# Kernel tuning notes

Measured on AMD Instinct MI355X. Metric: run time of the kernel, lower is better.

Reference implementation:

```python
import jax, jax.numpy as jnp
import numpy as np
from jax import lax

VOCAB = 32000; D = 1024; NL = 4; DI = 2048; S = 16; R = 64; DC = 4
B = 1; L = 1024; EPS = 1e-5


def setup_inputs() -> dict:
    key = jax.random.key(0)
    ks = jax.random.split(key, 16)
    def n(k, shape, s=0.02):
        return jax.random.normal(k, shape, dtype=jnp.float32) * s
    return dict(
        tokens=jax.random.randint(ks[0], (B, L), 0, VOCAB),
        embed=n(ks[1], (VOCAB, D)),
        norm_w=jnp.ones((NL, D), jnp.float32) + n(ks[2], (NL, D)),
        in_proj_w=n(ks[3], (NL, 2 * DI, D)),
        conv_w=n(ks[4], (NL, DI, DC), 0.1),
        conv_b=n(ks[5], (NL, DI)),
        x_proj_w=n(ks[6], (NL, R + 2 * S, DI)),
        dt_proj_w=n(ks[7], (NL, DI, R), 0.1),
        dt_proj_b=n(ks[8], (NL, DI), 0.5),
        A_log=n(ks[9], (NL, DI, S), 0.5),
        D_param=jnp.ones((NL, DI), jnp.float32) + n(ks[10], (NL, DI)),
        out_proj_w=n(ks[11], (NL, D, DI)),
        norm_f_w=jnp.ones((D,), jnp.float32),
        lm_head_w=n(ks[12], (VOCAB, D)),
    )


def _rmsnorm(x, w):
    return x * lax.rsqrt(jnp.mean(x * x, axis=-1, keepdims=True) + EPS) * w


def _mamba_block(x, norm_w, in_w, cw, cb, xw, dtw, dtb, a_log, dp, ow):
    # x: [B, L, D]
    res = x
    x = _rmsnorm(x, norm_w)
    xz = jnp.einsum('bld,ed->ble', x, in_w)      # [B, L, 2*DI]
    u, z = xz[..., :DI], xz[..., DI:]
    # depthwise causal conv over time
    u = jnp.swapaxes(u, 1, 2)                    # [B, DI, L]
    u = lax.conv_general_dilated(u, cw[:, None, :], (1,), [(DC - 1, 0)],
                                 feature_group_count=DI,
                                 dimension_numbers=('NCH', 'OIH', 'NCH'))
    u = jax.nn.silu(u + cb[None, :, None])
    u = jnp.swapaxes(u, 1, 2)                    # [B, L, DI]
    # input-dependent SSM params
    dbc = jnp.einsum('bld,ed->ble', u, xw)       # [B, L, R+2S]
    dt = jax.nn.softplus(jnp.einsum('blr,dr->bld', dbc[..., :R], dtw) + dtb)
    Bm = dbc[..., R:R + S]                       # [B, L, S]
    Cm = dbc[..., R + S:]                        # [B, L, S]
    A = -jnp.exp(a_log)                          # [DI, S]
    dA = jnp.exp(dt[..., None] * A)              # [B, L, DI, S]
    dBu = (dt * u)[..., None] * Bm[:, :, None, :]  # [B, L, DI, S]
    # selective scan over time
    def step(h, inp):
        a_t, b_t, c_t = inp
        h = a_t * h + b_t                        # [B, DI, S]
        y = jnp.einsum('bds,bs->bd', h, c_t)
        return h, y
    h0 = jnp.zeros((x.shape[0], DI, S), x.dtype)
    _, ys = lax.scan(step, h0, (jnp.moveaxis(dA, 1, 0), jnp.moveaxis(dBu, 1, 0), jnp.moveaxis(Cm, 1, 0)))
    y = jnp.moveaxis(ys, 0, 1) + u * dp          # [B, L, DI]
    y = y * jax.nn.silu(z)
    return res + jnp.einsum('bld,od->blo', y, ow)


def reference(tokens, embed, norm_w, in_proj_w, conv_w, conv_b, x_proj_w,
              dt_proj_w, dt_proj_b, A_log, D_param, out_proj_w, norm_f_w, lm_head_w):
    x = embed[tokens]                            # [B, L, D]
    for i in range(NL):
        x = _mamba_block(x, norm_w[i], in_proj_w[i], conv_w[i], conv_b[i],
                         x_proj_w[i], dt_proj_w[i], dt_proj_b[i], A_log[i],
                         D_param[i], out_proj_w[i])
    x = _rmsnorm(x, norm_f_w)
    return jnp.einsum('bld,vd->blv', x, lm_head_w)  # [B, L, VOCAB]
```

## Files before the change

### kernel.cpp

```cpp
#include <hip/hip_runtime.h>
#include <hip/hip_bf16.h>
#include <math.h>


typedef __attribute__((ext_vector_type(8))) short bf16x8;
typedef __attribute__((ext_vector_type(4))) float f32x4;

__device__ __forceinline__ short f2bf(float f) {
  union { float f; unsigned u; } v; v.f = f;
  unsigned u = v.u;
  unsigned r = (u + 0x7FFFu + ((u >> 16) & 1u)) >> 16;
  return (short)r;
}

__device__ __forceinline__ bf16x8 pack8(float4 a, float4 b) {
  bf16x8 r;
  r[0] = f2bf(a.x); r[1] = f2bf(a.y); r[2] = f2bf(a.z); r[3] = f2bf(a.w);
  r[4] = f2bf(b.x); r[5] = f2bf(b.y); r[6] = f2bf(b.z); r[7] = f2bf(b.w);
  return r;
}

__device__ __forceinline__ unsigned cvtpk(float lo, float hi) {
  unsigned r;
  asm("v_cvt_pk_bf16_f32 %0, %1, %2" : "=v"(r) : "v"(lo), "v"(hi));
  return r;
}

__device__ __forceinline__ float softplus_f(float x) {
  return (x > 20.f) ? x : log1pf(__expf(x));
}

__device__ __forceinline__ void gl_lds16(const void* g, void* l) {
  void* gnc = (void*)g;
  __builtin_amdgcn_global_load_lds((__attribute__((address_space(1))) void*)gnc,
                                   (__attribute__((address_space(3))) void*)l, 16, 0, 0);
}

__global__ __launch_bounds__(256) void cvt4_k(const float* __restrict__ s0, unsigned short* __restrict__ d0, int nb0,
                                              const float* __restrict__ s1, unsigned short* __restrict__ d1, int nb1,
                                              const float* __restrict__ s2, unsigned short* __restrict__ d2, int nb2,
                                              const float* __restrict__ s3, unsigned short* __restrict__ d3, int nb3) {
  int b = blockIdx.x;
  const float* s; unsigned short* d; int lb;
  if (b < nb0) { s = s0; d = d0; lb = b; }
  else if (b < nb0 + nb1) { s = s1; d = d1; lb = b - nb0; }
  else if (b < nb0 + nb1 + nb2) { s = s2; d = d2; lb = b - nb0 - nb1; }
  else { s = s3; d = d3; lb = b - nb0 - nb1 - nb2; }
  size_t base = (size_t)lb * 1024;
#pragma unroll
  for (int u = 0; u < 4; ++u) {
    size_t idx = base + u * 256 + threadIdx.x;
    const float4* p = (const float4*)(s + idx * 8);
    float4 a = p[0], bq = p[1];
    uint4 w;
    w.x = cvtpk(a.x, a.y); w.y = cvtpk(a.z, a.w);
    w.z = cvtpk(bq.x, bq.y); w.w = cvtpk(bq.z, bq.w);
    *(uint4*)(d + idx * 8) = w;
  }
}

__global__ __launch_bounds__(256) void embed_rms_k(const int* __restrict__ tok,
                                                   const float* __restrict__ emb,
                                                   const float* __restrict__ w,
                                                   float* __restrict__ x,
                                                   unsigned short* __restrict__ xn16) {
  int l = blockIdx.x;
  int t = tok[l];
  float4 v = ((const float4*)(emb + (size_t)t * 1024))[threadIdx.x];
  ((float4*)(x + (size_t)l * 1024))[threadIdx.x] = v;
  float ss = v.x * v.x + v.y * v.y + v.z * v.z + v.w * v.w;
  ss += __shfl_down(ss, 32); ss += __shfl_down(ss, 16); ss += __shfl_down(ss, 8);
  ss += __shfl_down(ss, 4);  ss += __shfl_down(ss, 2);  ss += __shfl_down(ss, 1);
  __shared__ float wsum[4];
  if ((threadIdx.x & 63) == 0) wsum[threadIdx.x >> 6] = ss;
  __syncthreads();
  float tot = wsum[0] + wsum[1] + wsum[2] + wsum[3];
  float sc = rsqrtf(tot * (1.0f / 1024.0f) + 1e-5f);
  float4 wv = ((const float4*)w)[threadIdx.x];
  ushort4 o;
  o.x = (unsigned short)f2bf(v.x * sc * wv.x);
  o.y = (unsigned short)f2bf(v.y * sc * wv.y);
  o.z = (unsigned short)f2bf(v.z * sc * wv.z);
  o.w = (unsigned short)f2bf(v.w * sc * wv.w);
  *(ushort4*)(xn16 + (size_t)l * 1024 + threadIdx.x * 4) = o;
}

__global__ __launch_bounds__(256) void rmsnorm16_k(const float* __restrict__ x,
                                                   const float* __restrict__ w,
                                                   unsigned short* __restrict__ y) {
  int l = blockIdx.x;
  const float4* xr = (const float4*)(x + (size_t)l * 1024);
  float4 v = xr[threadIdx.x];
  float ss = v.x * v.x + v.y * v.y + v.z * v.z + v.w * v.w;
  ss += __shfl_down(ss, 32); ss += __shfl_down(ss, 16); ss += __shfl_down(ss, 8);
  ss += __shfl_down(ss, 4);  ss += __shfl_down(ss, 2);  ss += __shfl_down(ss, 1);
  __shared__ float wsum[4];
  if ((threadIdx.x & 63) == 0) wsum[threadIdx.x >> 6] = ss;
  __syncthreads();
  float tot = wsum[0] + wsum[1] + wsum[2] + wsum[3];
  float sc = rsqrtf(tot * (1.0f / 1024.0f) + 1e-5f);
  float4 wv = ((const float4*)w)[threadIdx.x];
  ushort4 o;
  o.x = (unsigned short)f2bf(v.x * sc * wv.x);
  o.y = (unsigned short)f2bf(v.y * sc * wv.y);
  o.z = (unsigned short)f2bf(v.z * sc * wv.z);
  o.w = (unsigned short)f2bf(v.w * sc * wv.w);
  *(ushort4*)(y + (size_t)l * 1024 + threadIdx.x * 4) = o;
}

__global__ __launch_bounds__(256) void rmsnorm_k(const float* __restrict__ x,
                                                 const float* __restrict__ w,
                                                 float* __restrict__ y) {
  int l = blockIdx.x;
  const float4* xr = (const float4*)(x + (size_t)l * 1024);
  float4 v = xr[threadIdx.x];
  float ss = v.x * v.x + v.y * v.y + v.z * v.z + v.w * v.w;
  ss += __shfl_down(ss, 32); ss += __shfl_down(ss, 16); ss += __shfl_down(ss, 8);
  ss += __shfl_down(ss, 4);  ss += __shfl_down(ss, 2);  ss += __shfl_down(ss, 1);
  __shared__ float wsum[4];
  if ((threadIdx.x & 63) == 0) wsum[threadIdx.x >> 6] = ss;
  __syncthreads();
  float tot = wsum[0] + wsum[1] + wsum[2] + wsum[3];
  float sc = rsqrtf(tot * (1.0f / 1024.0f) + 1e-5f);
  float4 wv = ((const float4*)w)[threadIdx.x];
  float4 o;
  o.x = v.x * sc * wv.x; o.y = v.y * sc * wv.y;
  o.z = v.z * sc * wv.z; o.w = v.w * sc * wv.w;
  ((float4*)(y + (size_t)l * 1024))[threadIdx.x] = o;
}

__global__ __launch_bounds__(256) void conv_silu_k(const float* __restrict__ xz,
                                                   const float* __restrict__ cw,
                                                   const float* __restrict__ cb,
                                                   float* __restrict__ u,
                                                   unsigned short* __restrict__ u16) {
  int idx = blockIdx.x * 256 + threadIdx.x;
  int d = idx & 2047;
  int l = idx >> 11;
  float acc = cb[d];
#pragma unroll
  for (int j = 0; j < 4; ++j) {
    int ll = l - 3 + j;
    if (ll >= 0) acc = fmaf(xz[(size_t)ll * 4096 + d], cw[d * 4 + j], acc);
  }
  float sig = 1.0f / (1.0f + __expf(-acc));
  float v = acc * sig;
  u[idx] = v;
  if (u16) u16[idx] = (unsigned short)f2bf(v);
}

__global__ __launch_bounds__(256) void gemm16_k(const unsigned short* __restrict__ A, int lda,
                                                const unsigned short* __restrict__ W, int ldw,
                                                const float* __restrict__ addsrc,
                                                const float* __restrict__ spbias,
                                                float* __restrict__ C, int ldc,
                                                unsigned short* __restrict__ C16,
                                                int gx, int N, int K) {
  int total = gridDim.x;
  int lin = blockIdx.x;
  int q = total >> 3, r = total & 7;
  int xcd = lin & 7, idx = lin >> 3;
  int nl = (xcd < r ? xcd * (q + 1) : r * (q + 1) + (xcd - r) * q) + idx;
  const int bm = (nl % gx) << 7;
  const int bn = (nl / gx) << 7;

  const int tid = threadIdx.x;
  const int wid = tid >> 6;
  const int lane = tid & 63;
  const int wm = (wid >> 1) << 6;
  const int wn = (wid & 1) << 6;
  const int fr = lane & 15;
  const int kg = lane >> 4;
  const int srow = lane >> 3;
  const int sch  = lane & 7;
  const int xch  = sch ^ srow;

  __shared__ unsigned short sA[2][8192];
  __shared__ unsigned short sB[2][8192];

  f32x4 acc[4][4];
#pragma unroll
  for (int i = 0; i < 4; ++i)
#pragma unroll
    for (int j = 0; j < 4; ++j) acc[i][j] = (f32x4){0.f, 0.f, 0.f, 0.f};

  auto STAGE = [&](int b, int k0) {
#pragma unroll
    for (int t = 0; t < 4; ++t) {
      int g = (wid << 2) + t;
      int row = (g << 3) + srow;
      const unsigned short* ga = A + (size_t)(bm + row) * lda + k0 + (xch << 3);
      int wrow = bn + row; if (wrow >= N) wrow = N - 1;
      const unsigned short* gw = W + (size_t)wrow * ldw + k0 + (xch << 3);
      gl_lds16(ga, &sA[b][g << 9]);
      gl_lds16(gw, &sB[b][g << 9]);
    }
  };

  auto COMPUTE = [&](int b) {
#pragma unroll
    for (int ks = 0; ks < 2; ++ks) {
      bf16x8 af[4], bw[4];
#pragma unroll
      for (int mi = 0; mi < 4; ++mi) {
        int row = wm + (mi << 4) + fr;
        int xc = ((ks << 2) + kg) ^ (fr & 7);
        af[mi] = *(const bf16x8*)&sA[b][(row << 6) + (xc << 3)];
      }
#pragma unroll
      for (int ni = 0; ni < 4; ++ni) {
        int row = wn + (ni << 4) + fr;
        int xc = ((ks << 2) + kg) ^ (fr & 7);
        bw[ni] = *(const bf16x8*)&sB[b][(row << 6) + (xc << 3)];
      }
#pragma unroll
      for (int mi = 0; mi < 4; ++mi)
#pragma unroll
        for (int ni = 0; ni < 4; ++ni)
          acc[mi][ni] = __builtin_amdgcn_mfma_f32_16x16x32_bf16(af[mi], bw[ni], acc[mi][ni], 0, 0, 0);
    }
  };

  const int nt = K >> 6;
  STAGE(0, 0);
  int cur = 0;
  for (int t = 0; t + 1 < nt; ++t) {
    STAGE(cur ^ 1, (t + 1) << 6);
    asm volatile("s_waitcnt vmcnt(8)" ::: "memory");
    __builtin_amdgcn_s_barrier();
    __builtin_amdgcn_sched_barrier(0);
    COMPUTE(cur);
    __builtin_amdgcn_s_barrier();
    cur ^= 1;
  }
  asm volatile("s_waitcnt vmcnt(0)" ::: "memory");
  __builtin_amdgcn_s_barrier();
  __builtin_amdgcn_sched_barrier(0);
  COMPUTE(cur);

#pragma unroll
  for (int mi = 0; mi < 4; ++mi)
#pragma unroll
    for (int ni = 0; ni < 4; ++ni) {
      int n = bn + wn + (ni << 4) + fr;
      if (n < N) {
#pragma unroll
        for (int i = 0; i < 4; ++i) {
          int m = bm + wm + (mi << 4) + (kg << 2) + i;
          size_t off = (size_t)m * ldc + n;
          float v = acc[mi][ni][i];
          if (addsrc) v += addsrc[off];
          if (spbias) v = softplus_f(v + spbias[n]);
          C[off] = v;
          if (C16) C16[off] = (unsigned short)f2bf(v);
        }
      }
    }
}

__global__ __launch_bounds__(256) void gemm16sk_k(const unsigned short* __restrict__ A, int lda,
                                                  const unsigned short* __restrict__ W, int ldw,
                                                  float* __restrict__ Cp, int ldc,
                                                  int gx, int N, int Kchunk, int Mtot) {
  int total = gridDim.x;
  int lin = blockIdx.x;
  int q = total >> 3, r = total & 7;
  int xcd = lin & 7, idx = lin >> 3;
  int nl = (xcd < r ? xcd * (q + 1) : r * (q + 1) + (xcd - r) * q) + idx;
  const int bm = (nl % gx) << 7;
  const int bn = (nl / gx) << 7;
  const int ksplit = blockIdx.y;
  const int kbase = ksplit * Kchunk;

  const int tid = threadIdx.x;
  const int wid = tid >> 6;
  const int lane = tid & 63;
  const int wm = (wid >> 1) << 6;
  const int wn = (wid & 1) << 6;
  const int fr = lane & 15;
  const int kg = lane >> 4;
  const int srow = lane >> 3;
  const int sch  = lane & 7;
  const int xch  = sch ^ srow;

  __shared__ unsigned short sA[2][8192];
  __shared__ unsigned short sB[2][8192];

  f32x4 acc[4][4];
#pragma unroll
  for (int i = 0; i < 4; ++i)
#pragma unroll
    for (int j = 0; j < 4; ++j) acc[i][j] = (f32x4){0.f, 0.f, 0.f, 0.f};

  auto STAGE = [&](int b, int k0) {
#pragma unroll
    for (int t = 0; t < 4; ++t) {
      int g = (wid << 2) + t;
      int row = (g << 3) + srow;
      const unsigned short* ga = A + (size_t)(bm + row) * lda + k0 + (xch << 3);
      int wrow = bn + row; if (wrow >= N) wrow = N - 1;
      const unsigned short* gw = W + (size_t)wrow * ldw + k0 + (xch << 3);
      gl_lds16(ga, &sA[b][g << 9]);
      gl_lds16(gw, &sB[b][g << 9]);
    }
  };

  auto COMPUTE = [&](int b) {
#pragma unroll
    for (int ks = 0; ks < 2; ++ks) {
      bf16x8 af[4], bw[4];
#pragma unroll
      for (int mi = 0; mi < 4; ++mi) {
        int row = wm + (mi << 4) + fr;
        int xc = ((ks << 2) + kg) ^ (fr & 7);
        af[mi] = *(const bf16x8*)&sA[b][(row << 6) + (xc << 3)];
      }
#pragma unroll
      for (int ni = 0; ni < 4; ++ni) {
        int row = wn + (ni << 4) + fr;
        int xc = ((ks << 2) + kg) ^ (fr & 7);
        bw[ni] = *(const bf16x8*)&sB[b][(row << 6) + (xc << 3)];
      }
#pragma unroll
      for (int mi = 0; mi < 4; ++mi)
#pragma unroll
        for (int ni = 0; ni < 4; ++ni)
          acc[mi][ni] = __builtin_amdgcn_mfma_f32_16x16x32_bf16(af[mi], bw[ni], acc[mi][ni], 0, 0, 0);
    }
  };

  const int nt = Kchunk >> 6;
  STAGE(0, kbase);
  int cur = 0;
  for (int t = 0; t + 1 < nt; ++t) {
    STAGE(cur ^ 1, kbase + ((t + 1) << 6));
    asm volatile("s_waitcnt vmcnt(8)" ::: "memory");
    __builtin_amdgcn_s_barrier();
    __builtin_amdgcn_sched_barrier(0);
    COMPUTE(cur);
    __builtin_amdgcn_s_barrier();
    cur ^= 1;
  }
  asm volatile("s_waitcnt vmcnt(0)" ::: "memory");
  __builtin_amdgcn_s_barrier();
  __builtin_amdgcn_sched_barrier(0);
  COMPUTE(cur);

  float* Cs = Cp + (size_t)ksplit * Mtot * ldc;
#pragma unroll
  for (int mi = 0; mi < 4; ++mi)
#pragma unroll
    for (int ni = 0; ni < 4; ++ni) {
      int n = bn + wn + (ni << 4) + fr;
      if (n < N) {
#pragma unroll
        for (int i = 0; i < 4; ++i) {
          int m = bm + wm + (mi << 4) + (kg << 2) + i;
          Cs[(size_t)m * ldc + n] = acc[mi][ni][i];
        }
      }
    }
}

__global__ __launch_bounds__(256) void reduce_xp_k(const float* __restrict__ Cp,
                                                   float* __restrict__ dbc,
                                                   unsigned short* __restrict__ dbc16) {
  int i = blockIdx.x * 256 + threadIdx.x;
  float v = Cp[i] + Cp[98304 + i] + Cp[2 * 98304 + i] + Cp[3 * 98304 + i];
  dbc[i] = v;
  dbc16[i] = (unsigned short)f2bf(v);
}

__global__ __launch_bounds__(256) void reduce_op_k(const float* __restrict__ Cp,
                                                   float* __restrict__ x) {
  int i = blockIdx.x * 256 + threadIdx.x;
  const float4* p0 = (const float4*)Cp;
  const float4* p1 = (const float4*)(Cp + 1048576);
  const float4* p2 = (const float4*)(Cp + 2097152);
  const float4* p3 = (const float4*)(Cp + 3145728);
  float4 a = p0[i], b = p1[i], c = p2[i], d = p3[i];
  float4 xv = ((float4*)x)[i];
  xv.x += a.x + b.x + c.x + d.x;
  xv.y += a.y + b.y + c.y + d.y;
  xv.z += a.z + b.z + c.z + d.z;
  xv.w += a.w + b.w + c.w + d.w;
  ((float4*)x)[i] = xv;
}

struct WREG { float4 v[8]; };

__global__ __launch_bounds__(512, 2) void gemm256f_k(const unsigned short* __restrict__ A, int lda,
                                                     const float* __restrict__ W, int ldw,
                                                     float* __restrict__ C, int ldc,
                                                     int gx, int N, int K) {
  int total = gridDim.x;
  int lin = blockIdx.x;
  int q = total >> 3, r = total & 7;
  int xcd = lin & 7, idx = lin >> 3;
  int nl = (xcd < r ? xcd * (q + 1) : r * (q + 1) + (xcd - r) * q) + idx;
  const int bm = (nl % gx) << 8;
  const int bn = (nl / gx) << 8;

  const int tid = threadIdx.x;
  const int wid = tid >> 6;
  const int lane = tid & 63;
  const int wm = (wid >> 2) << 7;
  const int wn = (wid & 3) << 6;
  const int fr = lane & 15;
  const int kg = lane >> 4;
  const int srow = lane >> 3;
  const int sch  = lane & 7;
  const int xch  = sch ^ srow;

  const int wr_row  = tid >> 1;
  const int wr_half = tid & 1;
  int wr_grow = bn + wr_row; if (wr_grow >= N) wr_grow = N - 1;
  const float* gWrow = W + (size_t)wr_grow * ldw + wr_half * 32;

  __shared__ unsigned short sA[2][16384];
  __shared__ unsigned short sB[2][16384];

  f32x4 acc[8][4];
#pragma unroll
  for (int i = 0; i < 8; ++i)
#pragma unroll
    for (int j = 0; j < 4; ++j) acc[i][j] = (f32x4){0.f, 0.f, 0.f, 0.f};

  auto STAGE_A = [&](unsigned short* buf, int k0) {
#pragma unroll
    for (int t = 0; t < 4; ++t) {
      int g = (wid << 2) + t;
      int row = (g << 3) + srow;
      const unsigned short* ga = A + (size_t)(bm + row) * lda + k0 + (xch << 3);
      gl_lds16(ga, &buf[g << 9]);
    }
  };

  WREG wr;
  auto WLOAD = [&](int k0) {
    const float4* p = (const float4*)(gWrow + k0);
#pragma unroll
    for (int j = 0; j < 8; ++j) wr.v[j] = p[j];
  };

  auto WWRITE = [&](unsigned short* buf) {
#pragma unroll
    for (int c2 = 0; c2 < 4; ++c2) {
      int c = (wr_half << 2) + c2;
      uint4 val;
      val.x = cvtpk(wr.v[2 * c2].x,     wr.v[2 * c2].y);
      val.y = cvtpk(wr.v[2 * c2].z,     wr.v[2 * c2].w);
      val.z = cvtpk(wr.v[2 * c2 + 1].x, wr.v[2 * c2 + 1].y);
      val.w = cvtpk(wr.v[2 * c2 + 1].z, wr.v[2 * c2 + 1].w);
      *(uint4*)&buf[(wr_row << 6) + ((c ^ (wr_row & 7)) << 3)] = val;
    }
  };

  auto COMPUTE = [&](const unsigned short* bufa, const unsigned short* bufb) {
#pragma unroll
    for (int ks = 0; ks < 2; ++ks) {
      bf16x8 af[8], bw[4];
#pragma unroll
      for (int mi = 0; mi < 8; ++mi) {
        int row = wm + (mi << 4) + fr;
        int xc = ((ks << 2) + kg) ^ (fr & 7);
        af[mi] = *(const bf16x8*)&bufa[(row << 6) + (xc << 3)];
      }
#pragma unroll
      for (int ni = 0; ni < 4; ++ni) {
        int row = wn + (ni << 4) + fr;
        int xc = ((ks << 2) + kg) ^ (fr & 7);
        bw[ni] = *(const bf16x8*)&bufb[(row << 6) + (xc << 3)];
      }
#pragma unroll
      for (int mi = 0; mi < 8; ++mi)
#pragma unroll
        for (int ni = 0; ni < 4; ++ni)
          acc[mi][ni] = __builtin_amdgcn_mfma_f32_16x16x32_bf16(af[mi], bw[ni], acc[mi][ni], 0, 0, 0);
    }
  };

  const int nt = K >> 6;

  STAGE_A(sA[0], 0);
  WLOAD(0);
  asm volatile("s_waitcnt vmcnt(0)" ::: "memory");
  __builtin_amdgcn_sched_barrier(0);
  WWRITE(sB[0]);
  asm volatile("s_waitcnt lgkmcnt(0)" ::: "memory");
  __builtin_amdgcn_s_barrier();
  __builtin_amdgcn_sched_barrier(0);

  int cur = 0;
  for (int t = 0; t < nt; ++t) {
    if (t + 1 < nt) {
      STAGE_A(sA[cur ^ 1], (t + 1) << 6);
      WLOAD((t + 1) << 6);
      __builtin_amdgcn_sched_barrier(0);
    }
    COMPUTE(sA[cur], sB[cur]);
    __builtin_amdgcn_s_barrier();
    if (t + 1 < nt) {
      asm volatile("s_waitcnt vmcnt(0)" ::: "memory");
      __builtin_amdgcn_sched_barrier(0);
      WWRITE(sB[cur ^ 1]);
      asm volatile("s_waitcnt lgkmcnt(0)" ::: "memory");
      __builtin_amdgcn_s_barrier();
      __builtin_amdgcn_sched_barrier(0);
      cur ^= 1;
    }
  }

#pragma unroll
  for (int mi = 0; mi < 8; ++mi)
#pragma unroll
    for (int ni = 0; ni < 4; ++ni) {
      int n = bn + wn + (ni << 4) + fr;
      if (n < N) {
#pragma unroll
        for (int i = 0; i < 4; ++i) {
          int m = bm + wm + (mi << 4) + (kg << 2) + i;
          C[(size_t)m * ldc + n] = acc[mi][ni][i];
        }
      }
    }
}

__global__ __launch_bounds__(256) void gemm_bt_k(const float* __restrict__ A, int lda,
                                                 const float* __restrict__ W, int ldw,
                                                 const float* __restrict__ addsrc,
                                                 float* __restrict__ C, int ldc,
                                                 int N, int K) {
  const int tid  = threadIdx.x;
  const int srow = tid >> 1;
  const int skg  = (tid & 1) << 1;
  const int bm = blockIdx.x << 7;
  const int bn = blockIdx.y << 7;
  const int wid = tid >> 6;
  const int lane = tid & 63;
  const int wm = (wid >> 1) << 6;
  const int wn = (wid & 1) << 6;
  const int fr = lane & 15;
  const int kg = lane >> 4;

  __shared__ bf16x8 lA[4][128];
  __shared__ bf16x8 lB[4][128];

  f32x4 zero4 = {0.f, 0.f, 0.f, 0.f};
  f32x4 acc[4][4];
#pragma unroll
  for (int i = 0; i < 4; ++i)
#pragma unroll
    for (int j = 0; j < 4; ++j) acc[i][j] = zero4;

  const bool wvalid = (bn + srow) < N;
  const float* gA = A + (size_t)(bm + srow) * lda + (skg << 3);
  const float* gW = W + (size_t)(wvalid ? (bn + srow) : 0) * ldw + (skg << 3);

  for (int k0 = 0; k0 < K; k0 += 32) {
    float4 a0 = *(const float4*)(gA + k0);
    float4 a1 = *(const float4*)(gA + k0 + 4);
    float4 a2 = *(const float4*)(gA + k0 + 8);
    float4 a3 = *(const float4*)(gA + k0 + 12);
    float4 w0 = make_float4(0.f, 0.f, 0.f, 0.f), w1 = w0, w2 = w0, w3 = w0;
    if (wvalid) {
      w0 = *(const float4*)(gW + k0);
      w1 = *(const float4*)(gW + k0 + 4);
      w2 = *(const float4*)(gW + k0 + 8);
      w3 = *(const float4*)(gW + k0 + 12);
    }
    __syncthreads();
    lA[skg][srow]     = pack8(a0, a1);
    lA[skg + 1][srow] = pack8(a2, a3);
    lB[skg][srow]     = pack8(w0, w1);
    lB[skg + 1][srow] = pack8(w2, w3);
    __syncthreads();

    bf16x8 af[4], bf_[4];
#pragma unroll
    for (int mi = 0; mi < 4; ++mi) af[mi] = lA[kg][wm + (mi << 4) + fr];
#pragma unroll
    for (int ni = 0; ni < 4; ++ni) bf_[ni] = lB[kg][wn + (ni << 4) + fr];
#pragma unroll
    for (int mi = 0; mi < 4; ++mi)
#pragma unroll
      for (int ni = 0; ni < 4; ++ni)
        acc[mi][ni] = __builtin_amdgcn_mfma_f32_16x16x32_bf16(af[mi], bf_[ni], acc[mi][ni], 0, 0, 0);
  }

#pragma unroll
  for (int mi = 0; mi < 4; ++mi)
#pragma unroll
    for (int ni = 0; ni < 4; ++ni) {
      int n = bn + wn + (ni << 4) + fr;
      if (n < N) {
#pragma unroll
        for (int i = 0; i < 4; ++i) {
          int m = bm + wm + (mi << 4) + (kg << 2) + i;
          size_t off = (size_t)m * ldc + n;
          float v = acc[mi][ni][i];
          if (addsrc) v += addsrc[off];
          C[off] = v;
        }
      }
    }
}

#define NCH 32
#define CHL 32

__global__ __launch_bounds__(256) void scan_p1f_k(const float* __restrict__ dtv,
                                                  const float* __restrict__ u,
                                                  const float* __restrict__ dbc,
                                                  const float* __restrict__ A_log,
                                                  float* __restrict__ Pg,
                                                  float* __restrict__ qg) {
  int tid = threadIdx.x;
  int s = tid & 15, dg = tid >> 4;
  int d = (blockIdx.x << 4) + dg;
  int c = blockIdx.y;
  int l0 = c << 5;
  float A = -__expf(A_log[d * 16 + s]);
  float P = 1.f, q = 0.f;
#pragma unroll 4
  for (int i = 0; i < CHL; ++i) {
    int l = l0 + i;
    size_t rd = (size_t)l * 2048 + d;
    float dt = dtv[rd];
    float dA = __expf(dt * A);
    P *= dA;
    q = fmaf(dA, q, dt * u[rd] * dbc[l * 96 + 64 + s]);
  }
  size_t o = (size_t)c * 32768 + d * 16 + s;
  Pg[o] = P;
  qg[o] = q;
}

__global__ __launch_bounds__(256) void scan_p3f_k(const float* __restrict__ dtv,
                                                  const float* __restrict__ u,
                                                  const float* __restrict__ dbc,
                                                  const float* __restrict__ xz,
                                                  const float* __restrict__ A_log,
                                                  const float* __restrict__ Dp,
                                                  const float* __restrict__ Pg,
                                                  const float* __restrict__ qg,
                                                  unsigned short* __restrict__ y16) {
  int tid = threadIdx.x;
  int s = tid & 15, dg = tid >> 4;
  int d = (blockIdx.x << 4) + dg;
  int c = blockIdx.y;
  int l0 = c << 5;
  float A = -__expf(A_log[d * 16 + s]);
  float dpar = Dp[d];
  float h = 0.f;
  for (int cc = 0; cc < c; ++cc) {
    size_t o = (size_t)cc * 32768 + d * 16 + s;
    h = fmaf(Pg[o], h, qg[o]);
  }
#pragma unroll 4
  for (int i = 0; i < CHL; ++i) {
    int l = l0 + i;
    size_t rd = (size_t)l * 2048 + d;
    float dt = dtv[rd];
    float uv = u[rd];
    float dA = __expf(dt * A);
    h = fmaf(dA, h, dt * uv * dbc[l * 96 + 64 + s]);
    float p = h * dbc[l * 96 + 80 + s];
    p += __shfl_xor(p, 1); p += __shfl_xor(p, 2);
    p += __shfl_xor(p, 4); p += __shfl_xor(p, 8);
    if (s == 0) {
      float zv = xz[(size_t)l * 4096 + 2048 + d];
      float sig = 1.0f / (1.0f + __expf(-zv));
      y16[rd] = (unsigned short)f2bf((p + uv * dpar) * (zv * sig));
    }
  }
}

__global__ __launch_bounds__(256) void scan_p1_k(const float* __restrict__ dtr,
                                                 const float* __restrict__ u,
                                                 const float* __restrict__ dbc,
                                                 const float* __restrict__ A_log,
                                                 const float* __restrict__ dtb,
                                                 float* __restrict__ Pg,
                                                 float* __restrict__ qg) {
  int tid = threadIdx.x;
  int s = tid & 15, dg = tid >> 4;
  int d = (blockIdx.x << 4) + dg;
  int c = blockIdx.y;
  int l0 = c << 5;
  float A = -__expf(A_log[d * 16 + s]);
  float bias = dtb[d];
  float P = 1.f, q = 0.f;
#pragma unroll 4
  for (int i = 0; i < CHL; ++i) {
    int l = l0 + i;
    float dt = softplus_f(dtr[(size_t)l * 2048 + d] + bias);
    float dA = __expf(dt * A);
    P *= dA;
    q = fmaf(dA, q, dt * u[(size_t)l * 2048 + d] * dbc[l * 96 + 64 + s]);
  }
  size_t o = (size_t)c * 32768 + d * 16 + s;
  Pg[o] = P;
  qg[o] = q;
}

__global__ __launch_bounds__(256) void scan_p2_k(const float* __restrict__ Pg,
                                                 const float* __restrict__ qg,
                                                 float* __restrict__ hst) {
  int idx = blockIdx.x * 256 + threadIdx.x;
  float h = 0.f;
#pragma unroll
  for (int c = 0; c < NCH; ++c) {
    size_t o = (size_t)c * 32768 + idx;
    hst[o] = h;
    h = fmaf(Pg[o], h, qg[o]);
  }
}

__global__ __launch_bounds__(256) void scan_p3_k(const float* __restrict__ dtr,
                                                 const float* __restrict__ u,
                                                 const float* __restrict__ dbc,
                                                 const float* __restrict__ xz,
                                                 const float* __restrict__ A_log,
                                                 const float* __restrict__ Dp,
                                                 const float* __restrict__ dtb,
                                                 const float* __restrict__ hst,
                                                 float* __restrict__ y) {
  int tid = threadIdx.x;
  int s = tid & 15, dg = tid >> 4;
  int d = (blockIdx.x << 4) + dg;
  int c = blockIdx.y;
  int l0 = c << 5;
  float A = -__expf(A_log[d * 16 + s]);
  float dpar = Dp[d];
  float bias = dtb[d];
  float h = hst[(size_t)c * 32768 + d * 16 + s];
#pragma unroll 4
  for (int i = 0; i < CHL; ++i) {
    int l = l0 + i;
    size_t rd = (size_t)l * 2048 + d;
    float dt = softplus_f(dtr[rd] + bias);
    float uv = u[rd];
    float dA = __expf(dt * A);
    h = fmaf(dA, h, dt * uv * dbc[l * 96 + 64 + s]);
    float p = h * dbc[l * 96 + 80 + s];
    p += __shfl_xor(p, 1); p += __shfl_xor(p, 2);
    p += __shfl_xor(p, 4); p += __shfl_xor(p, 8);
    if (s == 0) {
      float zv = xz[(size_t)l * 4096 + 2048 + d];
      float sig = 1.0f / (1.0f + __expf(-zv));
      y[rd] = (p + uv * dpar) * (zv * sig);
    }
  }
}

extern "C" void kernel_launch(void* const* d_in, const int* in_sizes, int n_in,
                              void* d_out, int out_size, void* d_ws, size_t ws_size,
                              hipStream_t stream) {
  const int*   tokens = (const int*)d_in[0];
  const float* embed  = (const float*)d_in[1];
  const float* norm_w = (const float*)d_in[2];
  const float* in_w   = (const float*)d_in[3];
  const float* conv_w = (const float*)d_in[4];
  const float* conv_b = (const float*)d_in[5];
  const float* x_w    = (const float*)d_in[6];
  const float* dt_w   = (const float*)d_in[7];
  const float* dt_b   = (const float*)d_in[8];
  const float* A_log  = (const float*)d_in[9];
  const float* D_par  = (const float*)d_in[10];
  const float* out_w  = (const float*)d_in[11];
  const float* normf  = (const float*)d_in[12];
  const float* lm_w   = (const float*)d_in[13];

  float* out = (float*)d_out;
  float* x    = out;
  float* xz   = x    + 1024 * 1024;
  float* u    = xz   + 1024 * 4096;
  float* dtv  = u    + 1024 * 2048;
  float* dbc  = dtv  + 1024 * 2048;
  float* Pg   = dbc  + 1024 * 96;
  float* qg   = Pg   + 32 * 32768;
  float* hst  = qg   + 32 * 32768;
  float* xn_f = hst  + 32 * 32768;
  float* y_f  = xn_f + 1024 * 1024;
  unsigned short* xn16  = (unsigned short*)(y_f + 1024 * 2048);
  unsigned short* u16   = xn16 + 1024 * 1024;
  unsigned short* y16   = u16  + 1024 * 2048;
  unsigned short* dbc16 = y16  + 1024 * 2048;
  float* part_op = (float*)(dbc16 + 1024 * 96);
  float* part_xp = part_op + 4 * 1048576;

  unsigned short* inw16 = (unsigned short*)d_ws;
  unsigned short* oww16 = inw16 + 16777216;
  unsigned short* xw16  = oww16 + 8388608;
  unsigned short* dtw16 = xw16  + 786432;
  unsigned short* xnf16 = dtw16 + 524288;
  const size_t need = (size_t)(16777216 + 8388608 + 786432 + 524288 + 1048576) * 2;
  const bool fast = ws_size >= need;

  if (fast) {
    cvt4_k<<<3232, 256, 0, stream>>>(in_w, inw16, 2048,
                                     out_w, oww16, 1024,
                                     x_w, xw16, 96,
                                     dt_w, dtw16, 64);
    embed_rms_k<<<1024, 256, 0, stream>>>(tokens, embed, norm_w, x, xn16);

    for (int i = 0; i < 4; ++i) {
      if (i > 0) rmsnorm16_k<<<1024, 256, 0, stream>>>(x, norm_w + i * 1024, xn16);
      gemm16_k<<<256, 256, 0, stream>>>(xn16, 1024, inw16 + (size_t)i * 4194304, 1024,
                                        nullptr, nullptr, xz, 4096, nullptr, 8, 4096, 1024);
      conv_silu_k<<<8192, 256, 0, stream>>>(xz, conv_w + i * 8192, conv_b + i * 2048, u, u16);
      gemm16sk_k<<<dim3(8, 4), 256, 0, stream>>>(u16, 2048, xw16 + (size_t)i * 196608, 2048,
                                                 part_xp, 96, 8, 96, 512, 1024);
      reduce_xp_k<<<384, 256, 0, stream>>>(part_xp, dbc, dbc16);
      gemm16_k<<<128, 256, 0, stream>>>(dbc16, 96, dtw16 + (size_t)i * 131072, 64,
                                        nullptr, dt_b + i * 2048, dtv, 2048, nullptr, 8, 2048, 64);
      scan_p1f_k<<<dim3(128, NCH), 256, 0, stream>>>(dtv, u, dbc, A_log + i * 32768, Pg, qg);
      scan_p3f_k<<<dim3(128, NCH), 256, 0, stream>>>(dtv, u, dbc, xz, A_log + i * 32768,
                                                     D_par + i * 2048, Pg, qg, y16);
      gemm16sk_k<<<dim3(64, 4), 256, 0, stream>>>(y16, 2048, oww16 + (size_t)i * 2097152, 2048,
                                                  part_op, 1024, 8, 1024, 512, 1024);
      reduce_op_k<<<1024, 256, 0, stream>>>(part_op, x);
    }

    rmsnorm16_k<<<1024, 256, 0, stream>>>(x, normf, xnf16);
    gemm256f_k<<<500, 512, 0, stream>>>(xnf16, 1024, lm_w, 1024, out, 32000, 4, 32000, 1024);
  } else {
    float* xnf_f = (float*)d_ws;
    embed_rms_k<<<1024, 256, 0, stream>>>(tokens, embed, norm_w, x, xn16);
    for (int i = 0; i < 4; ++i) {
      rmsnorm_k<<<1024, 256, 0, stream>>>(x, norm_w + i * 1024, xn_f);
      gemm_bt_k<<<dim3(8, 32), 256, 0, stream>>>(xn_f, 1024, in_w + (size_t)i * 4194304, 1024,
                                                 nullptr, xz, 4096, 4096, 1024);
      conv_silu_k<<<8192, 256, 0, stream>>>(xz, conv_w + i * 8192, conv_b + i * 2048, u, nullptr);
      gemm_bt_k<<<dim3(8, 1), 256, 0, stream>>>(u, 2048, x_w + (size_t)i * 196608, 2048,
                                                nullptr, dbc, 96, 96, 2048);
      gemm_bt_k<<<dim3(8, 16), 256, 0, stream>>>(dbc, 96, dt_w + (size_t)i * 131072, 64,
                                                 nullptr, dtv, 2048, 2048, 64);
      scan_p1_k<<<dim3(128, NCH), 256, 0, stream>>>(dtv, u, dbc, A_log + i * 32768,
                                                    dt_b + i * 2048, Pg, qg);
      scan_p2_k<<<128, 256, 0, stream>>>(Pg, qg, hst);
      scan_p3_k<<<dim3(128, NCH), 256, 0, stream>>>(dtv, u, dbc, xz, A_log + i * 32768,
                                                    D_par + i * 2048, dt_b + i * 2048, hst, y_f);
      gemm_bt_k<<<dim3(8, 8), 256, 0, stream>>>(y_f, 2048, out_w + (size_t)i * 2097152, 2048,
                                                x, x, 1024, 1024, 2048);
    }
    rmsnorm_k<<<1024, 256, 0, stream>>>(x, normf, xnf_f);
    gemm_bt_k<<<dim3(8, 250), 256, 0, stream>>>(xnf_f, 1024, lm_w, 1024,
                                                nullptr, out, 32000, 32000, 1024);
  }
}
```

Before: 943.8 us.

## Pre-convert LM head weights to bf16 and triple-buffer the LM-head GEMM

```diff
diff --git a/kernel.cpp b/kernel.cpp
--- a/kernel.cpp
+++ b/kernel.cpp
@@ -387,12 +387,10 @@
   ((float4*)x)[i] = xv;
 }
 
-struct WREG { float4 v[8]; };
-
-__global__ __launch_bounds__(512, 2) void gemm256f_k(const unsigned short* __restrict__ A, int lda,
-                                                     const float* __restrict__ W, int ldw,
-                                                     float* __restrict__ C, int ldc,
-                                                     int gx, int N, int K) {
+__global__ __launch_bounds__(512, 2) void gemm256r3_k(const unsigned short* __restrict__ A, int lda,
+                                                      const unsigned short* __restrict__ W, int ldw,
+                                                      float* __restrict__ C, int ldc,
+                                                      int gx, int N, int K) {
   int total = gridDim.x;
   int lin = blockIdx.x;
   int q = total >> 3, r = total & 7;
@@ -408,17 +406,10 @@
   const int wn = (wid & 3) << 6;
   const int fr = lane & 15;
   const int kg = lane >> 4;
-  const int srow = lane >> 3;
-  const int sch  = lane & 7;
-  const int xch  = sch ^ srow;
-
-  const int wr_row  = tid >> 1;
-  const int wr_half = tid & 1;
-  int wr_grow = bn + wr_row; if (wr_grow >= N) wr_grow = N - 1;
-  const float* gWrow = W + (size_t)wr_grow * ldw + wr_half * 32;
-
-  __shared__ unsigned short sA[2][16384];
-  __shared__ unsigned short sB[2][16384];
+  const int lxch = (lane & 3) ^ ((lane >> 2) & 3) ^ ((lane >> 4) & 3);
+
+  __shared__ unsigned short sA[3][8192];
+  __shared__ unsigned short sB[3][8192];
 
   f32x4 acc[8][4];
 #pragma unroll
@@ -426,90 +417,63 @@
 #pragma unroll
     for (int j = 0; j < 4; ++j) acc[i][j] = (f32x4){0.f, 0.f, 0.f, 0.f};
 
-  auto STAGE_A = [&](unsigned short* buf, int k0) {
-#pragma unroll
-    for (int t = 0; t < 4; ++t) {
-      int g = (wid << 2) + t;
-      int row = (g << 3) + srow;
-      const unsigned short* ga = A + (size_t)(bm + row) * lda + k0 + (xch << 3);
-      gl_lds16(ga, &buf[g << 9]);
+  auto STAGE = [&](int b, int t) {
+    int k0 = t << 5;
+#pragma unroll
+    for (int i = 0; i < 2; ++i) {
+      int g = (wid << 1) + i;
+      int row = (g << 4) + (lane >> 2);
+      const unsigned short* ga = A + (size_t)(bm + row) * lda + k0 + (lxch << 3);
+      int wrow = bn + row; if (wrow >= N) wrow = N - 1;
+      const unsigned short* gw = W + (size_t)wrow * ldw + k0 + (lxch << 3);
+      gl_lds16(ga, &sA[b][g << 9]);
+      gl_lds16(gw, &sB[b][g << 9]);
     }
   };
 
-  WREG wr;
-  auto WLOAD = [&](int k0) {
-    const float4* p = (const float4*)(gWrow + k0);
-#pragma unroll
-    for (int j = 0; j < 8; ++j) wr.v[j] = p[j];
+  auto COMPUTE = [&](int b) {
+    bf16x8 af[8], bw[4];
+    const int xc = kg ^ (fr & 3) ^ (fr >> 2);
+#pragma unroll
+    for (int mi = 0; mi < 8; ++mi) {
+      int row = wm + (mi << 4) + fr;
+      af[mi] = *(const bf16x8*)&sA[b][(row << 5) + (xc << 3)];
+    }
+#pragma unroll
+    for (int ni = 0; ni < 4; ++ni) {
+      int row = wn + (ni << 4) + fr;
+      bw[ni] = *(const bf16x8*)&sB[b][(row << 5) + (xc << 3)];
+    }
+#pragma unroll
+    for (int mi = 0; mi < 8; ++mi)
+#pragma unroll
+      for (int ni = 0; ni < 4; ++ni)
+        acc[mi][ni] = __builtin_amdgcn_mfma_f32_16x16x32_bf16(af[mi], bw[ni], acc[mi][ni], 0, 0, 0);
   };
 
-  auto WWRITE = [&](unsigned short* buf) {
-#pragma unroll
-    for (int c2 = 0; c2 < 4; ++c2) {
-      int c = (wr_half << 2) + c2;
-      uint4 val;
-      val.x = cvtpk(wr.v[2 * c2].x,     wr.v[2 * c2].y);
-      val.y = cvtpk(wr.v[2 * c2].z,     wr.v[2 * c2].w);
-      val.z = cvtpk(wr.v[2 * c2 + 1].x, wr.v[2 * c2 + 1].y);
-      val.w = cvtpk(wr.v[2 * c2 + 1].z, wr.v[2 * c2 + 1].w);
-      *(uint4*)&buf[(wr_row << 6) + ((c ^ (wr_row & 7)) << 3)] = val;
-    }
-  };
-
-  auto COMPUTE = [&](const unsigned short* bufa, const unsigned short* bufb) {
-#pragma unroll
-    for (int ks = 0; ks < 2; ++ks) {
-      bf16x8 af[8], bw[4];
-#pragma unroll
-      for (int mi = 0; mi < 8; ++mi) {
-        int row = wm + (mi << 4) + fr;
-        int xc = ((ks << 2) + kg) ^ (fr & 7);
-        af[mi] = *(const bf16x8*)&bufa[(row << 6) + (xc << 3)];
-      }
-#pragma unroll
-      for (int ni = 0; ni < 4; ++ni) {
-        int row = wn + (ni << 4) + fr;
-        int xc = ((ks << 2) + kg) ^ (fr & 7);
-        bw[ni] = *(const bf16x8*)&bufb[(row << 6) + (xc << 3)];
-      }
-#pragma unroll
-      for (int mi = 0; mi < 8; ++mi)
-#pragma unroll
-        for (int ni = 0; ni < 4; ++ni)
-          acc[mi][ni] = __builtin_amdgcn_mfma_f32_16x16x32_bf16(af[mi], bw[ni], acc[mi][ni], 0, 0, 0);
-    }
-  };
-
-  const int nt = K >> 6;
-
-  STAGE_A(sA[0], 0);
-  WLOAD(0);
-  asm volatile("s_waitcnt vmcnt(0)" ::: "memory");
-  __builtin_amdgcn_sched_barrier(0);
-  WWRITE(sB[0]);
-  asm volatile("s_waitcnt lgkmcnt(0)" ::: "memory");
+  const int nt = K >> 5;
+  STAGE(0, 0); STAGE(1, 1); STAGE(2, 2);
+
+  int bi = 0;
+  for (int t = 0; t <= nt - 3; ++t) {
+    asm volatile("s_waitcnt vmcnt(8)" ::: "memory");
+    __builtin_amdgcn_s_barrier();
+    __builtin_amdgcn_sched_barrier(0);
+    COMPUTE(bi);
+    __builtin_amdgcn_s_barrier();
+    if (t + 3 < nt) STAGE(bi, t + 3);
+    bi = (bi == 2) ? 0 : bi + 1;
+  }
+  asm volatile("s_waitcnt vmcnt(4)" ::: "memory");
   __builtin_amdgcn_s_barrier();
   __builtin_amdgcn_sched_barrier(0);
-
-  int cur = 0;
-  for (int t = 0; t < nt; ++t) {
-    if (t + 1 < nt) {
-      STAGE_A(sA[cur ^ 1], (t + 1) << 6);
-      WLOAD((t + 1) << 6);
-      __builtin_amdgcn_sched_barrier(0);
-    }
-    COMPUTE(sA[cur], sB[cur]);
-    __builtin_amdgcn_s_barrier();
-    if (t + 1 < nt) {
-      asm volatile("s_waitcnt vmcnt(0)" ::: "memory");
-      __builtin_amdgcn_sched_barrier(0);
-      WWRITE(sB[cur ^ 1]);
-      asm volatile("s_waitcnt lgkmcnt(0)" ::: "memory");
-      __builtin_amdgcn_s_barrier();
-      __builtin_amdgcn_sched_barrier(0);
-      cur ^= 1;
-    }
-  }
+  COMPUTE(bi);
+  __builtin_amdgcn_s_barrier();
+  bi = (bi == 2) ? 0 : bi + 1;
+  asm volatile("s_waitcnt vmcnt(0)" ::: "memory");
+  __builtin_amdgcn_s_barrier();
+  __builtin_amdgcn_sched_barrier(0);
+  COMPUTE(bi);
 
 #pragma unroll
   for (int mi = 0; mi < 8; ++mi)
@@ -794,8 +758,9 @@
   unsigned short* oww16 = inw16 + 16777216;
   unsigned short* xw16  = oww16 + 8388608;
   unsigned short* dtw16 = xw16  + 786432;
-  unsigned short* xnf16 = dtw16 + 524288;
-  const size_t need = (size_t)(16777216 + 8388608 + 786432 + 524288 + 1048576) * 2;
+  unsigned short* lmw16 = dtw16 + 524288;
+  unsigned short* xnf16 = lmw16 + 32768000;
+  const size_t need = (size_t)(16777216 + 8388608 + 786432 + 524288 + 32768000 + 1048576) * 2;
   const bool fast = ws_size >= need;
 
   if (fast) {
@@ -803,6 +768,10 @@
                                      out_w, oww16, 1024,
                                      x_w, xw16, 96,
                                      dt_w, dtw16, 64);
+    cvt4_k<<<4000, 256, 0, stream>>>(lm_w, lmw16, 4000,
+                                     lm_w, lmw16, 0,
+                                     lm_w, lmw16, 0,
+                                     lm_w, lmw16, 0);
     embed_rms_k<<<1024, 256, 0, stream>>>(tokens, embed, norm_w, x, xn16);
 
     for (int i = 0; i < 4; ++i) {
@@ -824,7 +793,7 @@
     }
 
     rmsnorm16_k<<<1024, 256, 0, stream>>>(x, normf, xnf16);
-    gemm256f_k<<<500, 512, 0, stream>>>(xnf16, 1024, lm_w, 1024, out, 32000, 4, 32000, 1024);
+    gemm256r3_k<<<500, 512, 0, stream>>>(xnf16, 1024, lmw16, 1024, out, 32000, 4, 32000, 1024);
   } else {
     float* xnf_f = (float*)d_ws;
     embed_rms_k<<<1024, 256, 0, stream>>>(tokens, embed, norm_w, x, xn16);
```

Result: slower. 967.2 us (+2.5%).
